# Performance work log

Hardware: AMD Instinct MI355X
Metric: run time of the kernel (lower is better)

The kernel has to match this reference:

```python
import jax, jax.numpy as jnp
import numpy as np

N_NODES = 100000
N_EDGES = 1600000
D_IN = 128
D_HID = 128


def setup_inputs() -> dict:
    key = jax.random.key(0)
    ks = jax.random.split(key, 8)
    scale_in = 1.0 / np.sqrt(D_IN)
    scale_h = 1.0 / np.sqrt(D_HID)
    return {
        "x": jax.random.normal(ks[0], (N_NODES, D_IN), dtype=jnp.float32),
        "edge_index": jax.random.randint(ks[1], (2, N_EDGES), 0, N_NODES, dtype=jnp.int64),
        "W_l1": jax.random.normal(ks[2], (D_IN, D_HID), dtype=jnp.float32) * scale_in,
        "W_r1": jax.random.normal(ks[3], (D_IN, D_HID), dtype=jnp.float32) * scale_in,
        "b1": jnp.zeros((D_HID,), dtype=jnp.float32),
        "W_l2": jax.random.normal(ks[4], (D_HID, D_HID), dtype=jnp.float32) * scale_h,
        "W_r2": jax.random.normal(ks[5], (D_HID, D_HID), dtype=jnp.float32) * scale_h,
        "b2": jnp.zeros((D_HID,), dtype=jnp.float32),
    }


def _sage_conv(h, src, dst, n_nodes, W_l, W_r, b):
    # mean aggregation of source-node features onto destination nodes
    msg = h[src]                                         # [E, d] gather
    agg = jax.ops.segment_sum(msg, dst, num_segments=n_nodes)   # [N, d]
    cnt = jax.ops.segment_sum(jnp.ones((src.shape[0], 1), h.dtype), dst,
                              num_segments=n_nodes)      # [N, 1]
    mean = agg / jnp.maximum(cnt, 1.0)                   # zero where no in-edges
    return mean @ W_l + b + h @ W_r                      # lin_l(mean) + lin_r(x)


def reference(x, edge_index, W_l1, W_r1, b1, W_l2, W_r2, b2):
    src, dst = edge_index[0], edge_index[1]
    n = x.shape[0]
    h = jax.nn.relu(_sage_conv(x, src, dst, n, W_l1, W_r1, b1))
    # dropout is identity in eval mode
    return _sage_conv(h, src, dst, n, W_l2, W_r2, b2)
```

## Files before the change

### kernel.cpp

```cpp
#include <hip/hip_runtime.h>
#include <stdint.h>

#define N_NODES 100000
#define N_EDGES 1600000
#define D 128
#define NBUCK 196
#define BSTRIDE 9216
#define PCHUNK 2048
#define NTILE32 (N_NODES / 32)
#define CASTB 3125
#define WPACKB 128

typedef unsigned int uint32;
typedef __attribute__((ext_vector_type(8))) short short8;
typedef __attribute__((ext_vector_type(4))) float f32x4;

__device__ __forceinline__ unsigned short f2bf(float f) {
  unsigned u = __builtin_bit_cast(unsigned, f);
  u += 0x7fffu + ((u >> 16) & 1u);
  return (unsigned short)(u >> 16);
}
__device__ __forceinline__ float bflo(unsigned v) {
  return __builtin_bit_cast(float, v << 16);
}
__device__ __forceinline__ float bfhi(unsigned v) {
  return __builtin_bit_cast(float, v & 0xffff0000u);
}


__global__ __launch_bounds__(256) void k_part(const int* __restrict__ src,
                                              const int* __restrict__ dst,
                                              int* __restrict__ bcnt,
                                              uint2* __restrict__ pairs) {
  __shared__ uint2 buff[PCHUNK];
  __shared__ uint2 sorted[PCHUNK];
  __shared__ int hist[256], stmp[256], loff[256], cpos[256], base[256];
  int tid = threadIdx.x;
  int e0 = blockIdx.x * PCHUNK;
  int nv = N_EDGES - e0;
  if (nv > PCHUNK) nv = PCHUNK;

  hist[tid] = 0;
  __syncthreads();
  for (int i = tid; i < nv; i += 256) {
    int d = dst[e0 + i];
    int s = src[e0 + i];
    buff[i] = make_uint2((uint32)d, (uint32)s);
    atomicAdd(&hist[d >> 9], 1);
  }
  __syncthreads();
  int v = hist[tid];
  stmp[tid] = v;
  __syncthreads();
  for (int off = 1; off < 256; off <<= 1) {
    int t = (tid >= off) ? stmp[tid - off] : 0;
    __syncthreads();
    stmp[tid] += t;
    __syncthreads();
  }
  loff[tid] = stmp[tid] - v;
  cpos[tid] = stmp[tid] - v;
  base[tid] = (v > 0) ? atomicAdd(&bcnt[tid], v) : 0;
  __syncthreads();
  for (int i = tid; i < nv; i += 256) {
    uint2 p = buff[i];
    int r = atomicAdd(&cpos[p.x >> 9], 1);
    sorted[r] = p;
  }
  __syncthreads();
  for (int i = tid; i < nv; i += 256) {
    uint2 p = sorted[i];
    int b = (int)(p.x >> 9);
    int local = base[b] + (i - loff[b]);
    if (local < BSTRIDE)
      pairs[(size_t)b * BSTRIDE + local] = p;
  }
}

__global__ __launch_bounds__(512) void k_csr_prep(
    const uint2* __restrict__ pairs, const int* __restrict__ bcnt,
    int* __restrict__ rowptr, int* __restrict__ csr,
    const float* __restrict__ x, unsigned short* __restrict__ xb,
    const float* __restrict__ Wl1, const float* __restrict__ Wr1,
    const float* __restrict__ Wl2, const float* __restrict__ Wr2,
    unsigned short* __restrict__ Wp1, unsigned short* __restrict__ Wp2) {
  __shared__ int hist[512], off[512], cur[512], scn[512];
  int tid = threadIdx.x;
  int blk = blockIdx.x;

  if (blk >= NBUCK) {
    int pb = blk - NBUCK;
    if (pb < CASTB) {
      size_t i = (size_t)pb * 512 + tid;
      float4 a = *reinterpret_cast<const float4*>(x + i * 8);
      float4 c = *reinterpret_cast<const float4*>(x + i * 8 + 4);
      uint4 o;
      o.x = (uint32)f2bf(a.x) | ((uint32)f2bf(a.y) << 16);
      o.y = (uint32)f2bf(a.z) | ((uint32)f2bf(a.w) << 16);
      o.z = (uint32)f2bf(c.x) | ((uint32)f2bf(c.y) << 16);
      o.w = (uint32)f2bf(c.z) | ((uint32)f2bf(c.w) << 16);
      *reinterpret_cast<uint4*>(xb + i * 8) = o;
    } else {
      int t = (pb - CASTB) * 512 + tid;
      int which = t >> 15;
      int tt = t & 32767;
      int j = tt & 7;
      int lane = (tt >> 3) & 63;
      int tile = (tt >> 9) & 1;
      int ks = (tt >> 10) & 7;
      int ng = (tt >> 13) & 3;
      int k = ks * 32 + (lane >> 4) * 8 + j;
      int n = ng * 32 + tile * 16 + (lane & 15);
      const float* Wl = which ? Wl2 : Wl1;
      const float* Wr = which ? Wr2 : Wr1;
      float w = (k < 128) ? Wl[k * 128 + n] : Wr[(k - 128) * 128 + n];
      (which ? Wp2 : Wp1)[tt] = f2bf(w);
    }
    return;
  }

  int b = blk;
  int bv = (tid < NBUCK) ? bcnt[tid] : 0;
  scn[tid] = bv;
  __syncthreads();
  for (int o = 1; o < 512; o <<= 1) {
    int t = (tid >= o) ? scn[tid - o] : 0;
    __syncthreads();
    scn[tid] += t;
    __syncthreads();
  }
  int bb = (b == 0) ? 0 : scn[b - 1];
  if (b == NBUCK - 1 && tid == 0) rowptr[N_NODES] = scn[NBUCK - 1];

  int lo = b << 9;
  int hi = lo + 512;
  if (hi > N_NODES) hi = N_NODES;
  int ne = bcnt[b];
  if (ne > BSTRIDE) ne = BSTRIDE;
  const uint2* pb2 = pairs + (size_t)b * BSTRIDE;

  hist[tid] = 0;
  __syncthreads();
  for (int i = tid; i < ne; i += 512) atomicAdd(&hist[(int)pb2[i].x - lo], 1);
  __syncthreads();
  int v = hist[tid];
  off[tid] = v;
  __syncthreads();
  for (int o = 1; o < 512; o <<= 1) {
    int t = (tid >= o) ? off[tid - o] : 0;
    __syncthreads();
    off[tid] += t;
    __syncthreads();
  }
  off[tid] -= v;
  cur[tid] = off[tid];
  if (lo + tid < hi) rowptr[lo + tid] = bb + off[tid];
  __syncthreads();
  for (int i = tid; i < ne; i += 512) {
    int d = (int)pb2[i].x - lo;
    int slot = atomicAdd(&cur[d], 1);
    csr[bb + slot] = (int)pb2[i].y;
  }
}


#define ACC8(v)                                          \
  acc[0] += bflo(v.x); acc[1] += bfhi(v.x);              \
  acc[2] += bflo(v.y); acc[3] += bfhi(v.y);              \
  acc[4] += bflo(v.z); acc[5] += bfhi(v.z);              \
  acc[6] += bflo(v.w); acc[7] += bfhi(v.w);

__global__ __launch_bounds__(512, 4) void k_fused(
    const unsigned short* __restrict__ table,
    const int* __restrict__ rowptr, const int* __restrict__ csr,
    const unsigned short* __restrict__ Wp, const float* __restrict__ bias,
    void* __restrict__ outp, int relu_bf16_out) {
  __shared__ unsigned short meanB[32 * 128];
  int tid = threadIdx.x;
  int g = tid >> 4;
  int l = tid & 15;
  int tile = blockIdx.x;
  int node = tile * 32 + g;

  int beg = rowptr[node], end = rowptr[node + 1];
  float acc[8] = {0.f, 0.f, 0.f, 0.f, 0.f, 0.f, 0.f, 0.f};
  int e = beg;
  for (; e + 8 <= end; e += 8) {
    int s0 = csr[e], s1 = csr[e + 1], s2 = csr[e + 2], s3 = csr[e + 3];
    int s4 = csr[e + 4], s5 = csr[e + 5], s6 = csr[e + 6], s7 = csr[e + 7];
    uint4 v0 = *reinterpret_cast<const uint4*>(table + (size_t)s0 * D + l * 8);
    uint4 v1 = *reinterpret_cast<const uint4*>(table + (size_t)s1 * D + l * 8);
    uint4 v2 = *reinterpret_cast<const uint4*>(table + (size_t)s2 * D + l * 8);
    uint4 v3 = *reinterpret_cast<const uint4*>(table + (size_t)s3 * D + l * 8);
    uint4 v4 = *reinterpret_cast<const uint4*>(table + (size_t)s4 * D + l * 8);
    uint4 v5 = *reinterpret_cast<const uint4*>(table + (size_t)s5 * D + l * 8);
    uint4 v6 = *reinterpret_cast<const uint4*>(table + (size_t)s6 * D + l * 8);
    uint4 v7 = *reinterpret_cast<const uint4*>(table + (size_t)s7 * D + l * 8);
    ACC8(v0) ACC8(v1) ACC8(v2) ACC8(v3)
    ACC8(v4) ACC8(v5) ACC8(v6) ACC8(v7)
  }
  for (; e + 4 <= end; e += 4) {
    int s0 = csr[e], s1 = csr[e + 1], s2 = csr[e + 2], s3 = csr[e + 3];
    uint4 v0 = *reinterpret_cast<const uint4*>(table + (size_t)s0 * D + l * 8);
    uint4 v1 = *reinterpret_cast<const uint4*>(table + (size_t)s1 * D + l * 8);
    uint4 v2 = *reinterpret_cast<const uint4*>(table + (size_t)s2 * D + l * 8);
    uint4 v3 = *reinterpret_cast<const uint4*>(table + (size_t)s3 * D + l * 8);
    ACC8(v0) ACC8(v1) ACC8(v2) ACC8(v3)
  }
  for (; e < end; ++e) {
    int s0 = csr[e];
    uint4 v0 = *reinterpret_cast<const uint4*>(table + (size_t)s0 * D + l * 8);
    ACC8(v0)
  }
  float inv = (end > beg) ? 1.0f / (float)(end - beg) : 0.0f;
  uint4 o;
  o.x = (uint32)f2bf(acc[0] * inv) | ((uint32)f2bf(acc[1] * inv) << 16);
  o.y = (uint32)f2bf(acc[2] * inv) | ((uint32)f2bf(acc[3] * inv) << 16);
  o.z = (uint32)f2bf(acc[4] * inv) | ((uint32)f2bf(acc[5] * inv) << 16);
  o.w = (uint32)f2bf(acc[6] * inv) | ((uint32)f2bf(acc[7] * inv) << 16);
  *reinterpret_cast<uint4*>(&meanB[g * 128 + (l ^ (g & 15)) * 8]) = o;
  __syncthreads();

  int wave = tid >> 6;
  int lane = tid & 63;
  int wr = wave >> 2;
  int wc = wave & 3;
  int q = lane >> 4;
  int r = lane & 15;

  short8 Bf[8][2];
  const unsigned short* wp = Wp + (size_t)wc * 8192 + lane * 8;
#pragma unroll
  for (int ks = 0; ks < 8; ++ks)
#pragma unroll
    for (int t = 0; t < 2; ++t)
      Bf[ks][t] = *reinterpret_cast<const short8*>(wp + (ks * 2 + t) * 512);

  int arow = wr * 16 + r;
  short8 A[8];
  const unsigned short* ax = table + (size_t)(tile * 32 + arow) * D + q * 8;
#pragma unroll
  for (int ks = 0; ks < 4; ++ks)
    A[4 + ks] = *reinterpret_cast<const short8*>(ax + ks * 32);
#pragma unroll
  for (int ks = 0; ks < 4; ++ks) {
    int slot = (ks * 4 + q) ^ r;
    A[ks] = *reinterpret_cast<const short8*>(&meanB[arow * 128 + slot * 8]);
  }

  f32x4 c0 = {0.f, 0.f, 0.f, 0.f}, c1 = {0.f, 0.f, 0.f, 0.f};
#pragma unroll
  for (int ks = 0; ks < 8; ++ks) {
    c0 = __builtin_amdgcn_mfma_f32_16x16x32_bf16(A[ks], Bf[ks][0], c0, 0, 0, 0);
    c1 = __builtin_amdgcn_mfma_f32_16x16x32_bf16(A[ks], Bf[ks][1], c1, 0, 0, 0);
  }

  float bia0 = bias[wc * 32 + r];
  float bia1 = bias[wc * 32 + 16 + r];
  int orow = tile * 32 + wr * 16 + q * 4;
  if (relu_bf16_out) {
    unsigned short* ob = (unsigned short*)outp + (size_t)orow * D + wc * 32 + r;
#pragma unroll
    for (int gg = 0; gg < 4; ++gg) {
      ob[(size_t)gg * D] = f2bf(fmaxf(c0[gg] + bia0, 0.f));
      ob[(size_t)gg * D + 16] = f2bf(fmaxf(c1[gg] + bia1, 0.f));
    }
  } else {
    float* of = (float*)outp + (size_t)orow * D + wc * 32 + r;
#pragma unroll
    for (int gg = 0; gg < 4; ++gg) {
      of[(size_t)gg * D] = c0[gg] + bia0;
      of[(size_t)gg * D + 16] = c1[gg] + bia1;
    }
  }
}


extern "C" void kernel_launch(void* const* d_in, const int* in_sizes, int n_in,
                              void* d_out, int out_size, void* d_ws, size_t ws_size,
                              hipStream_t stream) {
  const float* x   = (const float*)d_in[0];
  const int*   ei  = (const int*)d_in[1];
  const float* Wl1 = (const float*)d_in[2];
  const float* Wr1 = (const float*)d_in[3];
  const float* b1  = (const float*)d_in[4];
  const float* Wl2 = (const float*)d_in[5];
  const float* Wr2 = (const float*)d_in[6];
  const float* b2  = (const float*)d_in[7];
  float* out = (float*)d_out;

  const int* esrc = ei;
  const int* edst = ei + N_EDGES;

  char* p = (char*)d_ws;
  auto take = [&](size_t bytes) {
    char* q = p;
    p += (bytes + 255) & ~(size_t)255;
    return q;
  };
  int* bcnt   = (int*)take(256 * 4);
  int* rowptr = (int*)take((size_t)(N_NODES + 1) * 4);
  int* csr    = (int*)take((size_t)N_EDGES * 4);
  uint2* pairs = (uint2*)take((size_t)NBUCK * BSTRIDE * 8);
  unsigned short* xb  = (unsigned short*)take((size_t)N_NODES * D * 2);
  unsigned short* hb  = (unsigned short*)take((size_t)N_NODES * D * 2);
  unsigned short* Wp1 = (unsigned short*)take(256 * 128 * 2);
  unsigned short* Wp2 = (unsigned short*)take(256 * 128 * 2);

  const int npart = (N_EDGES + PCHUNK - 1) / PCHUNK;

  hipMemsetAsync(bcnt, 0, 256 * 4, stream);
  k_part<<<npart, 256, 0, stream>>>(esrc, edst, bcnt, pairs);
  k_csr_prep<<<NBUCK + CASTB + WPACKB, 512, 0, stream>>>(
      pairs, bcnt, rowptr, csr, x, xb, Wl1, Wr1, Wl2, Wr2, Wp1, Wp2);

  k_fused<<<NTILE32, 512, 0, stream>>>(xb, rowptr, csr, Wp1, b1, hb, 1);
  k_fused<<<NTILE32, 512, 0, stream>>>(hb, rowptr, csr, Wp2, b2, out, 0);
}
```

Baseline: 319.0 us.

## Balance edge work across node groups in tile via packed dst-local csr and LDS atomics

Instead of one 16-thread group per destination node, each tile's edge range is split evenly across the 32 groups. The low 5 bits of the destination are packed into the top bits of each csr entry so a group can tell when it crosses into the next node. On each change it flushes its partial sums with shared-memory float atomics, and the mean is taken from LDS afterward. This targets load imbalance from varying in-degrees, at the cost of LDS atomics, an extra LDS buffer, extra barriers, and src ids limited to 27 bits.

```diff
diff --git a/kernel.cpp b/kernel.cpp
--- a/kernel.cpp
+++ b/kernel.cpp
@@ -10,6 +10,7 @@
 #define NTILE32 (N_NODES / 32)
 #define CASTB 3125
 #define WPACKB 128
+#define SRCMASK 0x07FFFFFFu
 
 typedef unsigned int uint32;
 typedef __attribute__((ext_vector_type(8))) short short8;
@@ -79,7 +80,7 @@
 
 __global__ __launch_bounds__(512) void k_csr_prep(
     const uint2* __restrict__ pairs, const int* __restrict__ bcnt,
-    int* __restrict__ rowptr, int* __restrict__ csr,
+    int* __restrict__ rowptr, uint32* __restrict__ csr,
     const float* __restrict__ x, unsigned short* __restrict__ xb,
     const float* __restrict__ Wl1, const float* __restrict__ Wr1,
     const float* __restrict__ Wl2, const float* __restrict__ Wr2,
@@ -159,7 +160,7 @@
   for (int i = tid; i < ne; i += 512) {
     int d = (int)pb2[i].x - lo;
     int slot = atomicAdd(&cur[d], 1);
-    csr[bb + slot] = (int)pb2[i].y;
+    csr[bb + slot] = (pb2[i].y & SRCMASK) | ((pb2[i].x & 31u) << 27);
   }
 }
 
@@ -170,55 +171,101 @@
   acc[4] += bflo(v.z); acc[5] += bfhi(v.z);              \
   acc[6] += bflo(v.w); acc[7] += bfhi(v.w);
 
+#define FLUSH8                                           \
+  { float* mrow = &meanS[cur * 128 + l * 8];             \
+    atomicAdd(mrow + 0, acc[0]); atomicAdd(mrow + 1, acc[1]); \
+    atomicAdd(mrow + 2, acc[2]); atomicAdd(mrow + 3, acc[3]); \
+    atomicAdd(mrow + 4, acc[4]); atomicAdd(mrow + 5, acc[5]); \
+    atomicAdd(mrow + 6, acc[6]); atomicAdd(mrow + 7, acc[7]); }
+
+#define GSTEP(p, v)                                      \
+  { int ld = (int)((p) >> 27);                           \
+    if (ld != cur) {                                     \
+      if (cur >= 0) FLUSH8                               \
+      cur = ld;                                          \
+      acc[0] = acc[1] = acc[2] = acc[3] = 0.f;           \
+      acc[4] = acc[5] = acc[6] = acc[7] = 0.f;           \
+    }                                                    \
+    ACC8(v) }
+
 __global__ __launch_bounds__(512, 4) void k_fused(
     const unsigned short* __restrict__ table,
-    const int* __restrict__ rowptr, const int* __restrict__ csr,
+    const int* __restrict__ rowptr, const uint32* __restrict__ csr,
     const unsigned short* __restrict__ Wp, const float* __restrict__ bias,
     void* __restrict__ outp, int relu_bf16_out) {
+  __shared__ float meanS[32 * 128];
+  __shared__ float invS[32];
   __shared__ unsigned short meanB[32 * 128];
   int tid = threadIdx.x;
-  int g = tid >> 4;
+  int g2 = tid >> 4;
   int l = tid & 15;
   int tile = blockIdx.x;
-  int node = tile * 32 + g;
-
-  int beg = rowptr[node], end = rowptr[node + 1];
+  int n0 = tile * 32;
+
+  {
+    float4 z = make_float4(0.f, 0.f, 0.f, 0.f);
+    *reinterpret_cast<float4*>(&meanS[tid * 8]) = z;
+    *reinterpret_cast<float4*>(&meanS[tid * 8 + 4]) = z;
+    if (tid < 32) {
+      int dg = rowptr[n0 + tid + 1] - rowptr[n0 + tid];
+      invS[tid] = (dg > 0) ? 1.0f / (float)dg : 0.0f;
+    }
+  }
+  int eb = rowptr[n0];
+  int ne = rowptr[n0 + 32] - eb;
+  int W = (ne + 31) >> 5;
+  int gb = eb + g2 * W;
+  int ge = gb + W;
+  int eend = eb + ne;
+  if (ge > eend) ge = eend;
+  __syncthreads();
+
   float acc[8] = {0.f, 0.f, 0.f, 0.f, 0.f, 0.f, 0.f, 0.f};
-  int e = beg;
-  for (; e + 8 <= end; e += 8) {
-    int s0 = csr[e], s1 = csr[e + 1], s2 = csr[e + 2], s3 = csr[e + 3];
-    int s4 = csr[e + 4], s5 = csr[e + 5], s6 = csr[e + 6], s7 = csr[e + 7];
-    uint4 v0 = *reinterpret_cast<const uint4*>(table + (size_t)s0 * D + l * 8);
-    uint4 v1 = *reinterpret_cast<const uint4*>(table + (size_t)s1 * D + l * 8);
-    uint4 v2 = *reinterpret_cast<const uint4*>(table + (size_t)s2 * D + l * 8);
-    uint4 v3 = *reinterpret_cast<const uint4*>(table + (size_t)s3 * D + l * 8);
-    uint4 v4 = *reinterpret_cast<const uint4*>(table + (size_t)s4 * D + l * 8);
-    uint4 v5 = *reinterpret_cast<const uint4*>(table + (size_t)s5 * D + l * 8);
-    uint4 v6 = *reinterpret_cast<const uint4*>(table + (size_t)s6 * D + l * 8);
-    uint4 v7 = *reinterpret_cast<const uint4*>(table + (size_t)s7 * D + l * 8);
-    ACC8(v0) ACC8(v1) ACC8(v2) ACC8(v3)
-    ACC8(v4) ACC8(v5) ACC8(v6) ACC8(v7)
-  }
-  for (; e + 4 <= end; e += 4) {
-    int s0 = csr[e], s1 = csr[e + 1], s2 = csr[e + 2], s3 = csr[e + 3];
-    uint4 v0 = *reinterpret_cast<const uint4*>(table + (size_t)s0 * D + l * 8);
-    uint4 v1 = *reinterpret_cast<const uint4*>(table + (size_t)s1 * D + l * 8);
-    uint4 v2 = *reinterpret_cast<const uint4*>(table + (size_t)s2 * D + l * 8);
-    uint4 v3 = *reinterpret_cast<const uint4*>(table + (size_t)s3 * D + l * 8);
-    ACC8(v0) ACC8(v1) ACC8(v2) ACC8(v3)
-  }
-  for (; e < end; ++e) {
-    int s0 = csr[e];
-    uint4 v0 = *reinterpret_cast<const uint4*>(table + (size_t)s0 * D + l * 8);
-    ACC8(v0)
-  }
-  float inv = (end > beg) ? 1.0f / (float)(end - beg) : 0.0f;
-  uint4 o;
-  o.x = (uint32)f2bf(acc[0] * inv) | ((uint32)f2bf(acc[1] * inv) << 16);
-  o.y = (uint32)f2bf(acc[2] * inv) | ((uint32)f2bf(acc[3] * inv) << 16);
-  o.z = (uint32)f2bf(acc[4] * inv) | ((uint32)f2bf(acc[5] * inv) << 16);
-  o.w = (uint32)f2bf(acc[6] * inv) | ((uint32)f2bf(acc[7] * inv) << 16);
-  *reinterpret_cast<uint4*>(&meanB[g * 128 + (l ^ (g & 15)) * 8]) = o;
+  int cur = -1;
+  int e = gb;
+  for (; e + 8 <= ge; e += 8) {
+    uint32 p0 = csr[e], p1 = csr[e + 1], p2 = csr[e + 2], p3 = csr[e + 3];
+    uint32 p4 = csr[e + 4], p5 = csr[e + 5], p6 = csr[e + 6], p7 = csr[e + 7];
+    uint4 v0 = *reinterpret_cast<const uint4*>(table + (size_t)(p0 & SRCMASK) * D + l * 8);
+    uint4 v1 = *reinterpret_cast<const uint4*>(table + (size_t)(p1 & SRCMASK) * D + l * 8);
+    uint4 v2 = *reinterpret_cast<const uint4*>(table + (size_t)(p2 & SRCMASK) * D + l * 8);
+    uint4 v3 = *reinterpret_cast<const uint4*>(table + (size_t)(p3 & SRCMASK) * D + l * 8);
+    uint4 v4 = *reinterpret_cast<const uint4*>(table + (size_t)(p4 & SRCMASK) * D + l * 8);
+    uint4 v5 = *reinterpret_cast<const uint4*>(table + (size_t)(p5 & SRCMASK) * D + l * 8);
+    uint4 v6 = *reinterpret_cast<const uint4*>(table + (size_t)(p6 & SRCMASK) * D + l * 8);
+    uint4 v7 = *reinterpret_cast<const uint4*>(table + (size_t)(p7 & SRCMASK) * D + l * 8);
+    GSTEP(p0, v0) GSTEP(p1, v1) GSTEP(p2, v2) GSTEP(p3, v3)
+    GSTEP(p4, v4) GSTEP(p5, v5) GSTEP(p6, v6) GSTEP(p7, v7)
+  }
+  for (; e + 4 <= ge; e += 4) {
+    uint32 p0 = csr[e], p1 = csr[e + 1], p2 = csr[e + 2], p3 = csr[e + 3];
+    uint4 v0 = *reinterpret_cast<const uint4*>(table + (size_t)(p0 & SRCMASK) * D + l * 8);
+    uint4 v1 = *reinterpret_cast<const uint4*>(table + (size_t)(p1 & SRCMASK) * D + l * 8);
+    uint4 v2 = *reinterpret_cast<const uint4*>(table + (size_t)(p2 & SRCMASK) * D + l * 8);
+    uint4 v3 = *reinterpret_cast<const uint4*>(table + (size_t)(p3 & SRCMASK) * D + l * 8);
+    GSTEP(p0, v0) GSTEP(p1, v1) GSTEP(p2, v2) GSTEP(p3, v3)
+  }
+  for (; e < ge; ++e) {
+    uint32 p0 = csr[e];
+    uint4 v0 = *reinterpret_cast<const uint4*>(table + (size_t)(p0 & SRCMASK) * D + l * 8);
+    GSTEP(p0, v0)
+  }
+  if (cur >= 0) FLUSH8
+  __syncthreads();
+
+  {
+    int row = tid >> 4;
+    int c8 = tid & 15;
+    float iv = invS[row];
+    float4 s0 = *reinterpret_cast<const float4*>(&meanS[row * 128 + c8 * 8]);
+    float4 s1 = *reinterpret_cast<const float4*>(&meanS[row * 128 + c8 * 8 + 4]);
+    uint4 o;
+    o.x = (uint32)f2bf(s0.x * iv) | ((uint32)f2bf(s0.y * iv) << 16);
+    o.y = (uint32)f2bf(s0.z * iv) | ((uint32)f2bf(s0.w * iv) << 16);
+    o.z = (uint32)f2bf(s1.x * iv) | ((uint32)f2bf(s1.y * iv) << 16);
+    o.w = (uint32)f2bf(s1.z * iv) | ((uint32)f2bf(s1.w * iv) << 16);
+    *reinterpret_cast<uint4*>(&meanB[row * 128 + (c8 ^ (row & 15)) * 8]) = o;
+  }
   __syncthreads();
 
   int wave = tid >> 6;
@@ -238,7 +285,7 @@
 
   int arow = wr * 16 + r;
   short8 A[8];
-  const unsigned short* ax = table + (size_t)(tile * 32 + arow) * D + q * 8;
+  const unsigned short* ax = table + (size_t)(n0 + arow) * D + q * 8;
 #pragma unroll
   for (int ks = 0; ks < 4; ++ks)
     A[4 + ks] = *reinterpret_cast<const short8*>(ax + ks * 32);
@@ -257,7 +304,7 @@
 
   float bia0 = bias[wc * 32 + r];
   float bia1 = bias[wc * 32 + 16 + r];
-  int orow = tile * 32 + wr * 16 + q * 4;
+  int orow = n0 + wr * 16 + q * 4;
   if (relu_bf16_out) {
     unsigned short* ob = (unsigned short*)outp + (size_t)orow * D + wc * 32 + r;
 #pragma unroll
@@ -300,7 +347,7 @@
   };
   int* bcnt   = (int*)take(256 * 4);
   int* rowptr = (int*)take((size_t)(N_NODES + 1) * 4);
-  int* csr    = (int*)take((size_t)N_EDGES * 4);
+  uint32* csr = (uint32*)take((size_t)N_EDGES * 4);
   uint2* pairs = (uint2*)take((size_t)NBUCK * BSTRIDE * 8);
   unsigned short* xb  = (unsigned short*)take((size_t)N_NODES * D * 2);
   unsigned short* hb  = (unsigned short*)take((size_t)N_NODES * D * 2);
```

Result: slower. 430.3 us (+34.9%).

## Shrink fused SAGE block to 128 threads with dynamic per-node work queue

Applied to the files above, without the earlier changes.

The fused aggregate+GEMM kernel now runs 128-thread blocks over 32-node tiles. Each 16-lane group pulls nodes from a shared-memory atomic counter instead of owning one fixed node, which balances degree skew inside the tile. The MFMA stage is restructured so each wave covers two 32-column output chunks across two 16-row tiles, loading weights per chunk instead of holding all of them in registers. This trades fewer threads per tile, and therefore fewer concurrent gathers per block, for better load balance and lower register pressure.

```diff
diff --git a/kernel.cpp b/kernel.cpp
--- a/kernel.cpp
+++ b/kernel.cpp
@@ -7,7 +7,8 @@
 #define NBUCK 196
 #define BSTRIDE 9216
 #define PCHUNK 2048
-#define NTILE32 (N_NODES / 32)
+#define QTILE 32
+#define NTILE (N_NODES / QTILE)
 #define CASTB 3125
 #define WPACKB 128
 
@@ -170,107 +171,125 @@
   acc[4] += bflo(v.z); acc[5] += bfhi(v.z);              \
   acc[6] += bflo(v.w); acc[7] += bfhi(v.w);
 
-__global__ __launch_bounds__(512, 4) void k_fused(
+__global__ __launch_bounds__(128, 6) void k_fused(
     const unsigned short* __restrict__ table,
     const int* __restrict__ rowptr, const int* __restrict__ csr,
     const unsigned short* __restrict__ Wp, const float* __restrict__ bias,
     void* __restrict__ outp, int relu_bf16_out) {
-  __shared__ unsigned short meanB[32 * 128];
+  __shared__ unsigned short meanB[QTILE * 128];
+  __shared__ int qS;
   int tid = threadIdx.x;
-  int g = tid >> 4;
+  int lane = tid & 63;
   int l = tid & 15;
-  int tile = blockIdx.x;
-  int node = tile * 32 + g;
-
-  int beg = rowptr[node], end = rowptr[node + 1];
-  float acc[8] = {0.f, 0.f, 0.f, 0.f, 0.f, 0.f, 0.f, 0.f};
-  int e = beg;
-  for (; e + 8 <= end; e += 8) {
-    int s0 = csr[e], s1 = csr[e + 1], s2 = csr[e + 2], s3 = csr[e + 3];
-    int s4 = csr[e + 4], s5 = csr[e + 5], s6 = csr[e + 6], s7 = csr[e + 7];
-    uint4 v0 = *reinterpret_cast<const uint4*>(table + (size_t)s0 * D + l * 8);
-    uint4 v1 = *reinterpret_cast<const uint4*>(table + (size_t)s1 * D + l * 8);
-    uint4 v2 = *reinterpret_cast<const uint4*>(table + (size_t)s2 * D + l * 8);
-    uint4 v3 = *reinterpret_cast<const uint4*>(table + (size_t)s3 * D + l * 8);
-    uint4 v4 = *reinterpret_cast<const uint4*>(table + (size_t)s4 * D + l * 8);
-    uint4 v5 = *reinterpret_cast<const uint4*>(table + (size_t)s5 * D + l * 8);
-    uint4 v6 = *reinterpret_cast<const uint4*>(table + (size_t)s6 * D + l * 8);
-    uint4 v7 = *reinterpret_cast<const uint4*>(table + (size_t)s7 * D + l * 8);
-    ACC8(v0) ACC8(v1) ACC8(v2) ACC8(v3)
-    ACC8(v4) ACC8(v5) ACC8(v6) ACC8(v7)
-  }
-  for (; e + 4 <= end; e += 4) {
-    int s0 = csr[e], s1 = csr[e + 1], s2 = csr[e + 2], s3 = csr[e + 3];
-    uint4 v0 = *reinterpret_cast<const uint4*>(table + (size_t)s0 * D + l * 8);
-    uint4 v1 = *reinterpret_cast<const uint4*>(table + (size_t)s1 * D + l * 8);
-    uint4 v2 = *reinterpret_cast<const uint4*>(table + (size_t)s2 * D + l * 8);
-    uint4 v3 = *reinterpret_cast<const uint4*>(table + (size_t)s3 * D + l * 8);
-    ACC8(v0) ACC8(v1) ACC8(v2) ACC8(v3)
-  }
-  for (; e < end; ++e) {
-    int s0 = csr[e];
-    uint4 v0 = *reinterpret_cast<const uint4*>(table + (size_t)s0 * D + l * 8);
-    ACC8(v0)
-  }
-  float inv = (end > beg) ? 1.0f / (float)(end - beg) : 0.0f;
-  uint4 o;
-  o.x = (uint32)f2bf(acc[0] * inv) | ((uint32)f2bf(acc[1] * inv) << 16);
-  o.y = (uint32)f2bf(acc[2] * inv) | ((uint32)f2bf(acc[3] * inv) << 16);
-  o.z = (uint32)f2bf(acc[4] * inv) | ((uint32)f2bf(acc[5] * inv) << 16);
-  o.w = (uint32)f2bf(acc[6] * inv) | ((uint32)f2bf(acc[7] * inv) << 16);
-  *reinterpret_cast<uint4*>(&meanB[g * 128 + (l ^ (g & 15)) * 8]) = o;
-  __syncthreads();
-
-  int wave = tid >> 6;
-  int lane = tid & 63;
-  int wr = wave >> 2;
-  int wc = wave & 3;
+  int n0 = blockIdx.x * QTILE;
+
+  if (tid == 0) qS = 0;
+  __syncthreads();
+
+  for (;;) {
+    int n;
+    if (l == 0) n = atomicAdd(&qS, 1);
+    n = __shfl(n, lane & 48);
+    if (n >= QTILE) break;
+    int node = n0 + n;
+    int beg = rowptr[node], end = rowptr[node + 1];
+    float acc[8] = {0.f, 0.f, 0.f, 0.f, 0.f, 0.f, 0.f, 0.f};
+    int e = beg;
+    for (; e + 8 <= end; e += 8) {
+      int s0 = csr[e], s1 = csr[e + 1], s2 = csr[e + 2], s3 = csr[e + 3];
+      int s4 = csr[e + 4], s5 = csr[e + 5], s6 = csr[e + 6], s7 = csr[e + 7];
+      uint4 v0 = *reinterpret_cast<const uint4*>(table + (size_t)s0 * D + l * 8);
+      uint4 v1 = *reinterpret_cast<const uint4*>(table + (size_t)s1 * D + l * 8);
+      uint4 v2 = *reinterpret_cast<const uint4*>(table + (size_t)s2 * D + l * 8);
+      uint4 v3 = *reinterpret_cast<const uint4*>(table + (size_t)s3 * D + l * 8);
+      uint4 v4 = *reinterpret_cast<const uint4*>(table + (size_t)s4 * D + l * 8);
+      uint4 v5 = *reinterpret_cast<const uint4*>(table + (size_t)s5 * D + l * 8);
+      uint4 v6 = *reinterpret_cast<const uint4*>(table + (size_t)s6 * D + l * 8);
+      uint4 v7 = *reinterpret_cast<const uint4*>(table + (size_t)s7 * D + l * 8);
+      ACC8(v0) ACC8(v1) ACC8(v2) ACC8(v3)
+      ACC8(v4) ACC8(v5) ACC8(v6) ACC8(v7)
+    }
+    for (; e + 4 <= end; e += 4) {
+      int s0 = csr[e], s1 = csr[e + 1], s2 = csr[e + 2], s3 = csr[e + 3];
+      uint4 v0 = *reinterpret_cast<const uint4*>(table + (size_t)s0 * D + l * 8);
+      uint4 v1 = *reinterpret_cast<const uint4*>(table + (size_t)s1 * D + l * 8);
+      uint4 v2 = *reinterpret_cast<const uint4*>(table + (size_t)s2 * D + l * 8);
+      uint4 v3 = *reinterpret_cast<const uint4*>(table + (size_t)s3 * D + l * 8);
+      ACC8(v0) ACC8(v1) ACC8(v2) ACC8(v3)
+    }
+    for (; e < end; ++e) {
+      int s0 = csr[e];
+      uint4 v0 = *reinterpret_cast<const uint4*>(table + (size_t)s0 * D + l * 8);
+      ACC8(v0)
+    }
+    float inv = (end > beg) ? 1.0f / (float)(end - beg) : 0.0f;
+    uint4 o;
+    o.x = (uint32)f2bf(acc[0] * inv) | ((uint32)f2bf(acc[1] * inv) << 16);
+    o.y = (uint32)f2bf(acc[2] * inv) | ((uint32)f2bf(acc[3] * inv) << 16);
+    o.z = (uint32)f2bf(acc[4] * inv) | ((uint32)f2bf(acc[5] * inv) << 16);
+    o.w = (uint32)f2bf(acc[6] * inv) | ((uint32)f2bf(acc[7] * inv) << 16);
+    *reinterpret_cast<uint4*>(&meanB[n * 128 + (l ^ (n & 15)) * 8]) = o;
+  }
+  __syncthreads();
+
+  int w = tid >> 6;
   int q = lane >> 4;
   int r = lane & 15;
 
-  short8 Bf[8][2];
-  const unsigned short* wp = Wp + (size_t)wc * 8192 + lane * 8;
-#pragma unroll
-  for (int ks = 0; ks < 8; ++ks)
-#pragma unroll
-    for (int t = 0; t < 2; ++t)
-      Bf[ks][t] = *reinterpret_cast<const short8*>(wp + (ks * 2 + t) * 512);
-
-  int arow = wr * 16 + r;
-  short8 A[8];
-  const unsigned short* ax = table + (size_t)(tile * 32 + arow) * D + q * 8;
-#pragma unroll
-  for (int ks = 0; ks < 4; ++ks)
-    A[4 + ks] = *reinterpret_cast<const short8*>(ax + ks * 32);
-#pragma unroll
-  for (int ks = 0; ks < 4; ++ks) {
-    int slot = (ks * 4 + q) ^ r;
-    A[ks] = *reinterpret_cast<const short8*>(&meanB[arow * 128 + slot * 8]);
-  }
-
-  f32x4 c0 = {0.f, 0.f, 0.f, 0.f}, c1 = {0.f, 0.f, 0.f, 0.f};
-#pragma unroll
-  for (int ks = 0; ks < 8; ++ks) {
-    c0 = __builtin_amdgcn_mfma_f32_16x16x32_bf16(A[ks], Bf[ks][0], c0, 0, 0, 0);
-    c1 = __builtin_amdgcn_mfma_f32_16x16x32_bf16(A[ks], Bf[ks][1], c1, 0, 0, 0);
-  }
-
-  float bia0 = bias[wc * 32 + r];
-  float bia1 = bias[wc * 32 + 16 + r];
-  int orow = tile * 32 + wr * 16 + q * 4;
-  if (relu_bf16_out) {
-    unsigned short* ob = (unsigned short*)outp + (size_t)orow * D + wc * 32 + r;
-#pragma unroll
-    for (int gg = 0; gg < 4; ++gg) {
-      ob[(size_t)gg * D] = f2bf(fmaxf(c0[gg] + bia0, 0.f));
-      ob[(size_t)gg * D + 16] = f2bf(fmaxf(c1[gg] + bia1, 0.f));
-    }
-  } else {
-    float* of = (float*)outp + (size_t)orow * D + wc * 32 + r;
-#pragma unroll
-    for (int gg = 0; gg < 4; ++gg) {
-      of[(size_t)gg * D] = c0[gg] + bia0;
-      of[(size_t)gg * D + 16] = c1[gg] + bia1;
+  for (int c = 0; c < 2; ++c) {
+    int cq = w * 2 + c;
+    float bia0 = bias[cq * 32 + r];
+    float bia1 = bias[cq * 32 + 16 + r];
+    const unsigned short* wp = Wp + (size_t)cq * 8192 + lane * 8;
+    for (int rt = 0; rt < 2; ++rt) {
+      int arow = rt * 16 + r;
+      f32x4 c0 = {0.f, 0.f, 0.f, 0.f}, c1 = {0.f, 0.f, 0.f, 0.f};
+      {
+        short8 A[4], B0[4], B1[4];
+#pragma unroll
+        for (int ks = 0; ks < 4; ++ks) {
+          int slot = (ks * 4 + q) ^ r;
+          A[ks] = *reinterpret_cast<const short8*>(&meanB[arow * 128 + slot * 8]);
+          B0[ks] = *reinterpret_cast<const short8*>(wp + (ks * 2 + 0) * 512);
+          B1[ks] = *reinterpret_cast<const short8*>(wp + (ks * 2 + 1) * 512);
+        }
+#pragma unroll
+        for (int ks = 0; ks < 4; ++ks) {
+          c0 = __builtin_amdgcn_mfma_f32_16x16x32_bf16(A[ks], B0[ks], c0, 0, 0, 0);
+          c1 = __builtin_amdgcn_mfma_f32_16x16x32_bf16(A[ks], B1[ks], c1, 0, 0, 0);
+        }
+      }
+      {
+        const unsigned short* ax = table + (size_t)(n0 + arow) * D + q * 8;
+        short8 A[4], B0[4], B1[4];
+#pragma unroll
+        for (int ks = 0; ks < 4; ++ks) {
+          A[ks] = *reinterpret_cast<const short8*>(ax + ks * 32);
+          B0[ks] = *reinterpret_cast<const short8*>(wp + ((ks + 4) * 2 + 0) * 512);
+          B1[ks] = *reinterpret_cast<const short8*>(wp + ((ks + 4) * 2 + 1) * 512);
+        }
+#pragma unroll
+        for (int ks = 0; ks < 4; ++ks) {
+          c0 = __builtin_amdgcn_mfma_f32_16x16x32_bf16(A[ks], B0[ks], c0, 0, 0, 0);
+          c1 = __builtin_amdgcn_mfma_f32_16x16x32_bf16(A[ks], B1[ks], c1, 0, 0, 0);
+        }
+      }
+      int orow = n0 + rt * 16 + q * 4;
+      if (relu_bf16_out) {
+        unsigned short* ob = (unsigned short*)outp + (size_t)orow * D + cq * 32 + r;
+#pragma unroll
+        for (int gg = 0; gg < 4; ++gg) {
+          ob[(size_t)gg * D] = f2bf(fmaxf(c0[gg] + bia0, 0.f));
+          ob[(size_t)gg * D + 16] = f2bf(fmaxf(c1[gg] + bia1, 0.f));
+        }
+      } else {
+        float* of = (float*)outp + (size_t)orow * D + cq * 32 + r;
+#pragma unroll
+        for (int gg = 0; gg < 4; ++gg) {
+          of[(size_t)gg * D] = c0[gg] + bia0;
+          of[(size_t)gg * D + 16] = c1[gg] + bia1;
+        }
+      }
     }
   }
 }
@@ -314,6 +333,6 @@
   k_csr_prep<<<NBUCK + CASTB + WPACKB, 512, 0, stream>>>(
       pairs, bcnt, rowptr, csr, x, xb, Wl1, Wr1, Wl2, Wr2, Wp1, Wp2);
 
-  k_fused<<<NTILE32, 512, 0, stream>>>(xb, rowptr, csr, Wp1, b1, hb, 1);
-  k_fused<<<NTILE32, 512, 0, stream>>>(hb, rowptr, csr, Wp2, b2, out, 0);
-}
+  k_fused<<<NTILE, 128, 0, stream>>>(xb, rowptr, csr, Wp1, b1, hb, 1);
+  k_fused<<<NTILE, 128, 0, stream>>>(hb, rowptr, csr, Wp2, b2, out, 0);
+}
```

After: 407.7 us. 27.8% more time.

## Reorder nodes by in-degree so each fused tile has balanced gather work

Applied to the files above, without the earlier changes.

Builds a histogram of node in-degrees while preparing the CSR, scans it, and writes a permutation that groups nodes by degree (capped at 63). The fused aggregate-plus-GEMM kernels then process nodes in this order, so the 16-lane groups in a block have similar edge counts and waves stall less on the longest row. The cost is two extra small kernels, indirect loads of the self-feature rows, scattered output row writes, and atomic-ordered slots that make node placement nondeterministic.

```diff
diff --git a/kernel.cpp b/kernel.cpp
--- a/kernel.cpp
+++ b/kernel.cpp
@@ -7,9 +7,12 @@
 #define NBUCK 196
 #define BSTRIDE 9216
 #define PCHUNK 2048
-#define NTILE32 (N_NODES / 32)
+#define QTILE 32
+#define NTILE (N_NODES / QTILE)
 #define CASTB 3125
 #define WPACKB 128
+#define DBINS 64
+#define ORDB 98
 
 typedef unsigned int uint32;
 typedef __attribute__((ext_vector_type(8))) short short8;
@@ -79,12 +82,12 @@
 
 __global__ __launch_bounds__(512) void k_csr_prep(
     const uint2* __restrict__ pairs, const int* __restrict__ bcnt,
-    int* __restrict__ rowptr, int* __restrict__ csr,
+    int* __restrict__ rowptr, int* __restrict__ csr, int* __restrict__ dhist,
     const float* __restrict__ x, unsigned short* __restrict__ xb,
     const float* __restrict__ Wl1, const float* __restrict__ Wr1,
     const float* __restrict__ Wl2, const float* __restrict__ Wr2,
     unsigned short* __restrict__ Wp1, unsigned short* __restrict__ Wp2) {
-  __shared__ int hist[512], off[512], cur[512], scn[512];
+  __shared__ int hist[512], off[512], cur[512], scn[512], dh[DBINS];
   int tid = threadIdx.x;
   int blk = blockIdx.x;
 
@@ -140,6 +143,7 @@
   const uint2* pb2 = pairs + (size_t)b * BSTRIDE;
 
   hist[tid] = 0;
+  if (tid < DBINS) dh[tid] = 0;
   __syncthreads();
   for (int i = tid; i < ne; i += 512) atomicAdd(&hist[(int)pb2[i].x - lo], 1);
   __syncthreads();
@@ -154,13 +158,43 @@
   }
   off[tid] -= v;
   cur[tid] = off[tid];
-  if (lo + tid < hi) rowptr[lo + tid] = bb + off[tid];
-  __syncthreads();
+  if (lo + tid < hi) {
+    rowptr[lo + tid] = bb + off[tid];
+    atomicAdd(&dh[v > 63 ? 63 : v], 1);
+  }
+  __syncthreads();
+  if (tid < DBINS && dh[tid]) atomicAdd(&dhist[tid], dh[tid]);
   for (int i = tid; i < ne; i += 512) {
     int d = (int)pb2[i].x - lo;
     int slot = atomicAdd(&cur[d], 1);
     csr[bb + slot] = (int)pb2[i].y;
   }
+}
+
+__global__ void k_dscan(const int* __restrict__ dhist, int* __restrict__ dbase) {
+  __shared__ int s[DBINS];
+  int t = threadIdx.x;
+  int v = dhist[t];
+  s[t] = v;
+  __syncthreads();
+  for (int o = 1; o < DBINS; o <<= 1) {
+    int x = (t >= o) ? s[t - o] : 0;
+    __syncthreads();
+    s[t] += x;
+    __syncthreads();
+  }
+  dbase[t] = s[t] - v;
+}
+
+__global__ __launch_bounds__(1024) void k_dorder(const int* __restrict__ rowptr,
+                                                 int* __restrict__ dbase,
+                                                 int* __restrict__ order) {
+  int n = blockIdx.x * 1024 + threadIdx.x;
+  if (n >= N_NODES) return;
+  int deg = rowptr[n + 1] - rowptr[n];
+  if (deg > 63) deg = 63;
+  int slot = atomicAdd(&dbase[deg], 1);
+  order[slot] = n;
 }
 
 
@@ -173,14 +207,15 @@
 __global__ __launch_bounds__(512, 4) void k_fused(
     const unsigned short* __restrict__ table,
     const int* __restrict__ rowptr, const int* __restrict__ csr,
+    const int* __restrict__ order,
     const unsigned short* __restrict__ Wp, const float* __restrict__ bias,
     void* __restrict__ outp, int relu_bf16_out) {
-  __shared__ unsigned short meanB[32 * 128];
+  __shared__ unsigned short meanB[QTILE * 128];
   int tid = threadIdx.x;
   int g = tid >> 4;
   int l = tid & 15;
-  int tile = blockIdx.x;
-  int node = tile * 32 + g;
+  int n0 = blockIdx.x * QTILE;
+  int node = order[n0 + g];
 
   int beg = rowptr[node], end = rowptr[node + 1];
   float acc[8] = {0.f, 0.f, 0.f, 0.f, 0.f, 0.f, 0.f, 0.f};
@@ -237,8 +272,9 @@
       Bf[ks][t] = *reinterpret_cast<const short8*>(wp + (ks * 2 + t) * 512);
 
   int arow = wr * 16 + r;
+  int an = order[n0 + arow];
   short8 A[8];
-  const unsigned short* ax = table + (size_t)(tile * 32 + arow) * D + q * 8;
+  const unsigned short* ax = table + (size_t)an * D + q * 8;
 #pragma unroll
   for (int ks = 0; ks < 4; ++ks)
     A[4 + ks] = *reinterpret_cast<const short8*>(ax + ks * 32);
@@ -257,20 +293,21 @@
 
   float bia0 = bias[wc * 32 + r];
   float bia1 = bias[wc * 32 + 16 + r];
-  int orow = tile * 32 + wr * 16 + q * 4;
   if (relu_bf16_out) {
-    unsigned short* ob = (unsigned short*)outp + (size_t)orow * D + wc * 32 + r;
 #pragma unroll
     for (int gg = 0; gg < 4; ++gg) {
-      ob[(size_t)gg * D] = f2bf(fmaxf(c0[gg] + bia0, 0.f));
-      ob[(size_t)gg * D + 16] = f2bf(fmaxf(c1[gg] + bia1, 0.f));
+      int on = order[n0 + wr * 16 + q * 4 + gg];
+      unsigned short* ob = (unsigned short*)outp + (size_t)on * D + wc * 32 + r;
+      ob[0] = f2bf(fmaxf(c0[gg] + bia0, 0.f));
+      ob[16] = f2bf(fmaxf(c1[gg] + bia1, 0.f));
     }
   } else {
-    float* of = (float*)outp + (size_t)orow * D + wc * 32 + r;
 #pragma unroll
     for (int gg = 0; gg < 4; ++gg) {
-      of[(size_t)gg * D] = c0[gg] + bia0;
-      of[(size_t)gg * D + 16] = c1[gg] + bia1;
+      int on = order[n0 + wr * 16 + q * 4 + gg];
+      float* of = (float*)outp + (size_t)on * D + wc * 32 + r;
+      of[0] = c0[gg] + bia0;
+      of[16] = c1[gg] + bia1;
     }
   }
 }
@@ -298,9 +335,13 @@
     p += (bytes + 255) & ~(size_t)255;
     return q;
   };
-  int* bcnt   = (int*)take(256 * 4);
+  int* ctrl   = (int*)take((256 + DBINS + DBINS) * 4);
+  int* bcnt   = ctrl;
+  int* dhist  = ctrl + 256;
+  int* dbase  = ctrl + 256 + DBINS;
   int* rowptr = (int*)take((size_t)(N_NODES + 1) * 4);
   int* csr    = (int*)take((size_t)N_EDGES * 4);
+  int* order  = (int*)take((size_t)N_NODES * 4);
   uint2* pairs = (uint2*)take((size_t)NBUCK * BSTRIDE * 8);
   unsigned short* xb  = (unsigned short*)take((size_t)N_NODES * D * 2);
   unsigned short* hb  = (unsigned short*)take((size_t)N_NODES * D * 2);
@@ -309,11 +350,13 @@
 
   const int npart = (N_EDGES + PCHUNK - 1) / PCHUNK;
 
-  hipMemsetAsync(bcnt, 0, 256 * 4, stream);
+  hipMemsetAsync(ctrl, 0, (256 + DBINS + DBINS) * 4, stream);
   k_part<<<npart, 256, 0, stream>>>(esrc, edst, bcnt, pairs);
   k_csr_prep<<<NBUCK + CASTB + WPACKB, 512, 0, stream>>>(
-      pairs, bcnt, rowptr, csr, x, xb, Wl1, Wr1, Wl2, Wr2, Wp1, Wp2);
-
-  k_fused<<<NTILE32, 512, 0, stream>>>(xb, rowptr, csr, Wp1, b1, hb, 1);
-  k_fused<<<NTILE32, 512, 0, stream>>>(hb, rowptr, csr, Wp2, b2, out, 0);
-}
+      pairs, bcnt, rowptr, csr, dhist, x, xb, Wl1, Wr1, Wl2, Wr2, Wp1, Wp2);
+  k_dscan<<<1, DBINS, 0, stream>>>(dhist, dbase);
+  k_dorder<<<ORDB, 1024, 0, stream>>>(rowptr, dbase, order);
+
+  k_fused<<<NTILE, 512, 0, stream>>>(xb, rowptr, csr, order, Wp1, b1, hb, 1);
+  k_fused<<<NTILE, 512, 0, stream>>>(hb, rowptr, csr, order, Wp2, b2, out, 0);
+}
```

Measured after the change: 568.9 us. 78.4% more time.
